# Kernel optimization log

Hardware: AMD Instinct MI355X
Metric: run time of the kernel (lower is better)

The kernel has to match this reference:

```python
import jax, jax.numpy as jnp
import numpy as np

N = 10000        # nodes
E = 160000       # edges (avg degree 16)
C = 64           # hidden channels
L = 2            # interaction/product/readout blocks
NTYPES = 5       # len(atomic_numbers)
NB = 8           # Bessel radial basis size
G = 100          # graphs in batch
R_MAX = 5.0
AVG_NEI = 16.0   # avg_num_neighbors normalization
LM = 9           # (l_max+1)^2, l_max=2


def _spherical_harmonics(u):
    # real spherical harmonics up to l=2 of unit vectors u [E,3] -> [E,9]
    x, y, z = u[:, 0], u[:, 1], u[:, 2]
    s3 = 1.7320508
    one = jnp.ones_like(x)
    return jnp.stack([
        one,                       # l=0
        x, y, z,                   # l=1
        s3 * x * y,                # l=2
        s3 * y * z,
        0.5 * (3.0 * z * z - 1.0),
        s3 * x * z,
        0.5 * s3 * (x * x - y * y),
    ], axis=-1)


def _radial_embedding(r):
    # Bessel basis * polynomial cutoff (p=6); r [E] -> [E,NB]
    r_safe = jnp.maximum(r, 1e-9)
    n = jnp.arange(1, NB + 1, dtype=r.dtype)
    pref = jnp.sqrt(jnp.asarray(2.0 / R_MAX, r.dtype))
    bessel = pref * jnp.sin(n[None, :] * jnp.pi * r[:, None] / R_MAX) / r_safe[:, None]
    xx = r / R_MAX
    env = 1.0 - 28.0 * xx**6 + 48.0 * xx**7 - 21.0 * xx**8
    env = jnp.where(xx < 1.0, env, 0.0)
    return bessel * env[:, None]


def setup_inputs() -> dict:
    key = jax.random.key(0)
    ks = jax.random.split(key, 14)
    sc = 0.1
    return {
        'pos': jax.random.normal(ks[0], (N, 3), jnp.float32),
        'W_embed': jax.random.normal(ks[1], (NTYPES, C), jnp.float32) * sc,
        'W_r1': jax.random.normal(ks[2], (NB, 64), jnp.float32) * sc,
        'b_r1': jnp.zeros((64,), jnp.float32),
        'W_r2': jax.random.normal(ks[3], (64, C), jnp.float32) * sc,
        'W_up': jax.random.normal(ks[4], (L, C, C), jnp.float32) * sc,
        'W_sc': jax.random.normal(ks[5], (L, C, C), jnp.float32) * sc,
        'W_prod': jax.random.normal(ks[6], (L, C, C), jnp.float32) * sc,
        'w_ro': jax.random.normal(ks[7], (L, C, 1), jnp.float32) * sc,
        'atom_types': jax.random.randint(ks[8], (N,), 0, NTYPES),
        'edge_index': jax.random.randint(ks[9], (2, E), 0, N),
        'batch': jnp.sort(jax.random.randint(ks[10], (N,), 0, G)),
        'num_graphs': G,
    }


def reference(pos, W_embed, W_r1, b_r1, W_r2, W_up, W_sc, W_prod, w_ro,
              atom_types, edge_index, batch, num_graphs):
    node_attrs = jax.nn.one_hot(atom_types, NTYPES, dtype=pos.dtype)   # [N,5]
    h = node_attrs @ W_embed                                           # [N,C]

    sender, receiver = edge_index[0], edge_index[1]
    vec = pos[receiver] - pos[sender]                                  # edge gather
    r = jnp.linalg.norm(vec, axis=-1)                                  # [E]
    u = vec / jnp.maximum(r, 1e-9)[:, None]
    sh = _spherical_harmonics(u)                                       # [E,LM]
    ef = _radial_embedding(r)                                          # [E,NB]
    R = jax.nn.silu(ef @ W_r1 + b_r1) @ W_r2                            # [E,C] radial MLP

    pair_energy = jnp.zeros((num_graphs,), pos.dtype)                  # no pair_repulsion_fn
    energies = [pair_energy]
    for l in range(L):
        h1 = h @ W_up[l]                                               # [N,C]
        # tensor-product message: outer(sh_e, R_e * h_sender)  [E,LM,C]
        m = sh[:, :, None] * (R * h1[sender])[:, None, :]
        A = jax.ops.segment_sum(m, receiver, num_segments=N) / AVG_NEI  # [N,LM,C]
        sc = h @ W_sc[l]                                               # skip connection
        # product basis: l=0 channel + quadratic invariant contraction
        q = A[:, 0, :] + jnp.sum(A * A, axis=1)                         # [N,C]
        h = q @ W_prod[l] + sc
        node_e = (h @ w_ro[l])[:, 0]                                    # [N]
        energies.append(jax.ops.segment_sum(node_e, batch, num_segments=num_graphs))

    contributions = jnp.stack(energies, axis=-1)                        # [G, L+1]
    total_energy = jnp.sum(contributions, axis=-1)                      # [G]
    return total_energy
```

## Files before the change

kernel.cpp:

```cpp
#include <hip/hip_runtime.h>
#include <hip/hip_fp16.h>
#include <math.h>

#define Nn 10000
#define Ee 160000
#define NBb 8
#define Gg 100
#define NT 5
#define CSRMAX 230400
#define EDGEBLK (CSRMAX / 256)

typedef _Float16 half8v __attribute__((ext_vector_type(8)));
typedef float f32x4v __attribute__((ext_vector_type(4)));

__device__ __align__(16) float g_shc[(size_t)CSRMAX * 12];
__device__ __align__(16) __half2 g_R2[(size_t)(CSRMAX / 2) * 64];
__device__ float g_h1a[Nn * 64];
__device__ float g_h1b[Nn * 64];
__device__ float g_hscb[Nn * 64];
__device__ float g_nodeE[2][Nn];
__device__ int   g_deg[Nn];
__device__ int   g_offs[Nn + 1];
__device__ int   g_cursor[Nn];
__device__ int2  g_er[CSRMAX];
__device__ float g_W1T[64 * NBb];
__device__ float g_E1[NT * 64];
__device__ float g_Esc[NT * 64];
__device__ float g_T1[NT * 64];
__device__ float g_T2[NT * 64];
__device__ float g_M12[64 * 128];
__device__ float g_wp0ro[64];
__device__ float g_wpro[64];
__device__ float g_t0[NT];

__global__ __launch_bounds__(256) void k_init(const float* __restrict__ Wr1,
                                              const float* __restrict__ Wembed,
                                              const float* __restrict__ Wup,
                                              const float* __restrict__ Wsc,
                                              const float* __restrict__ Wprod,
                                              const float* __restrict__ wro,
                                              float* __restrict__ out, int out_size) {
    int t = threadIdx.x;
    int b = blockIdx.x;
    if (b >= 17) {
        int i = (b - 17) * 256 + t;
        if (i < CSRMAX) g_er[i].x = -1;
        if (i < out_size) out[i] = 0.0f;
        if (i < Nn) { g_deg[i] = 0; g_cursor[i] = 0; }
        return;
    }
    if (b == 0) {
        for (int i = t; i < 64 * NBb; i += 256) {
            int k = i >> 6, j = i & 63;
            g_W1T[j * NBb + k] = Wr1[i];
        }
        for (int i = t; i < NT * 64; i += 256) {
            int g = i >> 6, c = i & 63;
            float s1 = 0.f, s2 = 0.f;
            for (int j = 0; j < 64; j++) {
                float w = Wembed[g * 64 + j];
                s1 += w * Wup[j * 64 + c];
                s2 += w * Wsc[j * 64 + c];
            }
            g_E1[i] = s1; g_Esc[i] = s2;
        }
        if (t < 64) {
            float s1 = 0.f, s2 = 0.f;
            for (int c = 0; c < 64; c++) {
                s1 += Wprod[t * 64 + c] * wro[c];
                s2 += Wprod[4096 + t * 64 + c] * wro[64 + c];
            }
            g_wp0ro[t] = s1; g_wpro[t] = s2;
        }
        __syncthreads();
        for (int i = t; i < NT * 64; i += 256) {
            int g = i >> 6, c = i & 63;
            float s1 = 0.f, s2 = 0.f;
            for (int j = 0; j < 64; j++) {
                float w = g_Esc[g * 64 + j];
                s1 += w * Wup[4096 + j * 64 + c];
                s2 += w * Wsc[4096 + j * 64 + c];
            }
            g_T1[i] = s1; g_T2[i] = s2;
        }
        if (t < NT) {
            float s = 0.f;
            for (int j = 0; j < 64; j++) s += g_Esc[t * 64 + j] * wro[j];
            g_t0[t] = s;
        }
    } else {
        int idx = (b - 1) * 256 + t;
        int k = idx >> 6, c = idx & 63;
        float s1 = 0.f, s2 = 0.f;
        for (int j = 0; j < 64; j++) {
            float w = Wprod[k * 64 + j];
            s1 += w * Wup[4096 + j * 64 + c];
            s2 += w * Wsc[4096 + j * 64 + c];
        }
        g_M12[k * 128 + c] = s1;
        g_M12[k * 128 + 64 + c] = s2;
    }
}

__global__ __launch_bounds__(256) void k_deg(const int* __restrict__ eidx) {
    int e = blockIdx.x * 256 + threadIdx.x;
    if (e < Ee) atomicAdd(&g_deg[eidx[Ee + e]], 1);
}

__global__ __launch_bounds__(1024) void k_scan() {
    __shared__ int part[1024];
    int t = threadIdx.x;
    const int CH = (Nn + 1023) / 1024;
    int st = t * CH;
    int en = st + CH; if (en > Nn) en = Nn;
    int s = 0;
    for (int i = st; i < en; i++) s += (g_deg[i] + 7) & ~7;
    part[t] = s;
    __syncthreads();
    for (int d = 1; d < 1024; d <<= 1) {
        int v = (t >= d) ? part[t - d] : 0;
        __syncthreads();
        part[t] += v;
        __syncthreads();
    }
    int base = (t == 0) ? 0 : part[t - 1];
    for (int i = st; i < en; i++) { g_offs[i] = base; base += (g_deg[i] + 7) & ~7; }
    if (t == 1023) g_offs[Nn] = part[1023];
}

__global__ __launch_bounds__(256) void k_fill(const int* __restrict__ eidx) {
    int e = blockIdx.x * 256 + threadIdx.x;
    if (e >= Ee) return;
    int snd = eidx[e];
    int r = eidx[Ee + e];
    int p = g_offs[r] + atomicAdd(&g_cursor[r], 1);
    g_er[p] = make_int2(snd, r);
}

__global__ __launch_bounds__(256) void k_edge(const float* __restrict__ pos,
                                              const float* __restrict__ br1,
                                              const float* __restrict__ Wr2,
                                              const int* __restrict__ atom_types) {
    int t = threadIdx.x;
    if (blockIdx.x >= EDGEBLK) {
        int i = (blockIdx.x - EDGEBLK) * 256 + t;
        if (i < Nn * 64) {
            int n = i >> 6, c = i & 63;
            g_h1a[i] = g_E1[atom_types[n] * 64 + c];
        }
        return;
    }
    __shared__ _Float16 sA[256 * 64];
    __shared__ _Float16 sB[64 * 64];
    int total = g_offs[Nn];
    if (blockIdx.x * 256 >= total) return;

    for (int i = t; i < 64 * 64; i += 256)
        sB[(i & 63) * 64 + (i >> 6)] = (_Float16)Wr2[i];

    int s = blockIdx.x * 256 + t;
    int2 er = g_er[s];
    bool real = (er.x >= 0);
    int snd = real ? er.x : 0;
    int rcv = real ? er.y : 0;

    float vx = pos[3 * rcv + 0] - pos[3 * snd + 0];
    float vy = pos[3 * rcv + 1] - pos[3 * snd + 1];
    float vz = pos[3 * rcv + 2] - pos[3 * snd + 2];
    float r = sqrtf(vx * vx + vy * vy + vz * vz);
    float inv = __builtin_amdgcn_rcpf(fmaxf(r, 1e-9f));
    float x = vx * inv, y = vy * inv, z = vz * inv;
    const float s3 = 1.7320508f;
    {
        float4* shp = (float4*)(g_shc + (size_t)s * 12);
        if (real) {
            shp[0] = make_float4(1.0f, x, y, z);
            shp[1] = make_float4(s3 * x * y, s3 * y * z, 0.5f * (3.0f * z * z - 1.0f), s3 * x * z);
            shp[2] = make_float4(0.5f * s3 * (x * x - y * y), __int_as_float(snd), 0.f, 0.f);
        } else {
            shp[0] = make_float4(0.f, 0.f, 0.f, 0.f);
            shp[1] = make_float4(0.f, 0.f, 0.f, 0.f);
            shp[2] = make_float4(0.f, 0.f, 0.f, 0.f);
        }
    }

    float xx = r * 0.2f;
    float env = 0.0f;
    if (xx < 1.0f) {
        float x2 = xx * xx;
        float x6 = x2 * x2 * x2;
        float x7 = x6 * xx;
        float x8 = x7 * xx;
        env = 1.0f - 28.0f * x6 + 48.0f * x7 - 21.0f * x8;
    }
    const float pref = 0.63245553f;
    const float PI_F = 3.14159265358979f;
    float fac = pref * inv * env;
    float ef[NBb];
#pragma unroll
    for (int k = 0; k < NBb; k++)
        ef[k] = fac * __sinf((float)(k + 1) * PI_F * r * 0.2f);

#pragma unroll
    for (int gnl = 0; gnl < 8; gnl++) {
        half8v h8;
#pragma unroll
        for (int i2 = 0; i2 < 8; i2++) {
            int j = gnl * 8 + i2;
            float a = br1[j];
#pragma unroll
            for (int k = 0; k < NBb; k++) a += ef[k] * g_W1T[j * NBb + k];
            a = a * __builtin_amdgcn_rcpf(1.0f + __expf(-a));
            h8[i2] = (_Float16)(real ? a : 0.0f);
        }
        int pg = gnl ^ (t & 7);
        *(half8v*)&sA[t * 64 + pg * 8] = h8;
    }
    __syncthreads();

    int lane = t & 63;
    int w = t >> 6;
    half8v Bf[4][2];
#pragma unroll
    for (int n = 0; n < 4; n++) {
#pragma unroll
        for (int kk = 0; kk < 2; kk++) {
            int c = n * 16 + (lane & 15);
            int j0 = kk * 32 + (lane >> 4) * 8;
            Bf[n][kk] = *(const half8v*)&sB[c * 64 + j0];
        }
    }
#pragma unroll
    for (int m = 0; m < 4; m++) {
        int row = w * 64 + m * 16 + (lane & 15);
        int q0 = (lane >> 4) ^ (lane & 7);
        int q1 = (4 + (lane >> 4)) ^ (lane & 7);
        half8v A0 = *(const half8v*)&sA[row * 64 + q0 * 8];
        half8v A1 = *(const half8v*)&sA[row * 64 + q1 * 8];
        size_t pairbase = (size_t)blockIdx.x * 128 + (size_t)w * 32 + m * 8 + (lane >> 4) * 2;
        int cbase = lane & 15;
#pragma unroll
        for (int n = 0; n < 4; n++) {
            f32x4v d = {0.f, 0.f, 0.f, 0.f};
            d = __builtin_amdgcn_mfma_f32_16x16x32_f16(A0, Bf[n][0], d, 0, 0, 0);
            d = __builtin_amdgcn_mfma_f32_16x16x32_f16(A1, Bf[n][1], d, 0, 0, 0);
            int c = n * 16 + cbase;
            g_R2[pairbase * 64 + c]       = __floats2half2_rn(d[0], d[1]);
            g_R2[(pairbase + 1) * 64 + c] = __floats2half2_rn(d[2], d[3]);
        }
    }
}

#define NODE_BATCH(j0)                                                           \
    {                                                                            \
        const float* __restrict__ rp = g_shc + (size_t)(j0) * 12;                \
        __half2 r2[4];                                                           \
        _Pragma("unroll")                                                        \
        for (int kk = 0; kk < 4; kk++)                                           \
            r2[kk] = g_R2[((j0) / 2 + kk) * 64 + lane];                          \
        float s8v[8]; int srcv[8];                                               \
        _Pragma("unroll")                                                        \
        for (int k = 0; k < 8; k++) {                                            \
            float2 rc = *(const float2*)(rp + k * 12 + 8);                       \
            s8v[k] = rc.x; srcv[k] = __float_as_int(rc.y);                       \
        }                                                                        \
        float hv[8];                                                             \
        _Pragma("unroll")                                                        \
        for (int k = 0; k < 8; k++)                                              \
            hv[k] = hsrc[(size_t)srcv[k] * 64 + lane];                           \
        _Pragma("unroll")                                                        \
        for (int k = 0; k < 8; k++) {                                            \
            float4 ra = *(const float4*)(rp + k * 12);                           \
            float4 rb = *(const float4*)(rp + k * 12 + 4);                       \
            float rv = (k & 1) ? __high2float(r2[k >> 1]) : __low2float(r2[k >> 1]); \
            float tv = rv * hv[k];                                               \
            A[0] += ra.x * tv; A[1] += ra.y * tv; A[2] += ra.z * tv;             \
            A[3] += ra.w * tv; A[4] += rb.x * tv; A[5] += rb.y * tv;             \
            A[6] += rb.z * tv; A[7] += rb.w * tv; A[8] += s8v[k] * tv;           \
        }                                                                        \
    }

__global__ __launch_bounds__(256) void k_node0(const int* __restrict__ atom_types) {
    int t = threadIdx.x;
    int node = blockIdx.x * 4 + (t >> 6);
    int lane = t & 63;
    int boff = __builtin_amdgcn_readfirstlane(g_offs[node]);
    int nb = (__builtin_amdgcn_readfirstlane(g_deg[node]) + 7) >> 3;
    const float* __restrict__ hsrc = g_h1a;
    float A[9];
#pragma unroll
    for (int m = 0; m < 9; m++) A[m] = 0.0f;
#pragma unroll
    for (int b = 0; b < 4; b++)
        if (b < nb) NODE_BATCH((size_t)boff + (size_t)b * 8);
    for (int b = 4; b < nb; b++) {
        size_t j0 = (size_t)boff + (size_t)b * 8;
        NODE_BATCH(j0);
    }
    const float invn = 1.0f / 16.0f;
    float q = A[0] * invn;
#pragma unroll
    for (int m = 0; m < 9; m++) {
        float a = A[m] * invn;
        q += a * a;
    }
    int type = __builtin_amdgcn_readfirstlane(atom_types[node]);
    float h1n = g_T1[type * 64 + lane];
    float hscn = g_T2[type * 64 + lane];
#pragma unroll
    for (int k = 0; k < 64; k++) {
        float qk = __shfl(q, k, 64);
        h1n += qk * g_M12[k * 128 + lane];
        hscn += qk * g_M12[k * 128 + 64 + lane];
    }
    g_h1b[node * 64 + lane] = h1n;
    g_hscb[node * 64 + lane] = hscn;
    float v = q * g_wp0ro[lane];
#pragma unroll
    for (int off = 32; off > 0; off >>= 1) v += __shfl_down(v, off, 64);
    if (lane == 0) g_nodeE[0][node] = v + g_t0[type];
}

__global__ __launch_bounds__(256) void k_node1(const float* __restrict__ wro) {
    int t = threadIdx.x;
    int node = blockIdx.x * 4 + (t >> 6);
    int lane = t & 63;
    int boff = __builtin_amdgcn_readfirstlane(g_offs[node]);
    int nb = (__builtin_amdgcn_readfirstlane(g_deg[node]) + 7) >> 3;
    const float* __restrict__ hsrc = g_h1b;
    float A[9];
#pragma unroll
    for (int m = 0; m < 9; m++) A[m] = 0.0f;
#pragma unroll
    for (int b = 0; b < 4; b++)
        if (b < nb) NODE_BATCH((size_t)boff + (size_t)b * 8);
    for (int b = 4; b < nb; b++) {
        size_t j0 = (size_t)boff + (size_t)b * 8;
        NODE_BATCH(j0);
    }
    const float invn = 1.0f / 16.0f;
    float q = A[0] * invn;
#pragma unroll
    for (int m = 0; m < 9; m++) {
        float a = A[m] * invn;
        q += a * a;
    }
    float v = q * g_wpro[lane] + g_hscb[node * 64 + lane] * wro[lane];
#pragma unroll
    for (int off = 32; off > 0; off >>= 1) v += __shfl_down(v, off, 64);
    if (lane == 0) g_nodeE[1][node] = v;
}

__global__ __launch_bounds__(64) void k_energy(const int* __restrict__ batch,
                                               float* __restrict__ out) {
    int g = blockIdx.x;
    int lane = threadIdx.x;
    int a = 0, b = Nn;
    while (a < b) { int m = (a + b) >> 1; if (batch[m] < g) a = m + 1; else b = m; }
    int st = a;
    b = Nn;
    while (a < b) { int m = (a + b) >> 1; if (batch[m] < g + 1) a = m + 1; else b = m; }
    int en = a;
    float s = 0.0f;
    for (int i = st + lane; i < en; i += 64) s += g_nodeE[0][i] + g_nodeE[1][i];
#pragma unroll
    for (int off = 32; off > 0; off >>= 1) s += __shfl_down(s, off, 64);
    if (lane == 0) out[g] = s;
}

extern "C" void kernel_launch(void* const* d_in, const int* in_sizes, int n_in,
                              void* d_out, int out_size, void* d_ws, size_t ws_size,
                              hipStream_t stream) {
    const float* pos     = (const float*)d_in[0];
    const float* W_embed = (const float*)d_in[1];
    const float* W_r1    = (const float*)d_in[2];
    const float* b_r1    = (const float*)d_in[3];
    const float* W_r2    = (const float*)d_in[4];
    const float* W_up    = (const float*)d_in[5];
    const float* W_sc    = (const float*)d_in[6];
    const float* W_prod  = (const float*)d_in[7];
    const float* w_ro    = (const float*)d_in[8];
    const int* atom_types = (const int*)d_in[9];
    const int* eidx       = (const int*)d_in[10];
    const int* batch      = (const int*)d_in[11];
    float* out = (float*)d_out;

    k_init<<<17 + EDGEBLK, 256, 0, stream>>>(W_r1, W_embed, W_up, W_sc, W_prod, w_ro, out, out_size);
    k_deg<<<Ee / 256, 256, 0, stream>>>(eidx);
    k_scan<<<1, 1024, 0, stream>>>();
    k_fill<<<Ee / 256, 256, 0, stream>>>(eidx);
    k_edge<<<EDGEBLK + (Nn * 64 + 255) / 256, 256, 0, stream>>>(pos, b_r1, W_r2, atom_types);
    k_node0<<<Nn / 4, 256, 0, stream>>>(atom_types);
    k_node1<<<Nn / 4, 256, 0, stream>>>(w_ro + 64);
    k_energy<<<Gg, 64, 0, stream>>>(batch, out);
}
```

Baseline: 189.0 us.

## Pretranspose W_r2 once, batch node gathers ahead of compute, cap node occupancy

A new small kernel converts W_r2 to a transposed fp16 global buffer once, so each edge block loads its MFMA B fragments from global memory instead of rebuilding a shared-memory copy. The node kernels now issue all gather loads for the first four 8-edge batches before doing any accumulation, giving more memory-level parallelism at the cost of more registers. Launch bounds are tightened to four blocks per SM. k_init also gains a strange branch for block 1 that writes dummy values to the same buffer, which k_w2t then overwrites. That branch is harmless only because of stream ordering.

```diff
diff --git a/kernel.cpp b/kernel.cpp
--- a/kernel.cpp
+++ b/kernel.cpp
@@ -24,6 +24,7 @@
 __device__ int   g_cursor[Nn];
 __device__ int2  g_er[CSRMAX];
 __device__ float g_W1T[64 * NBb];
+__device__ __align__(16) _Float16 g_W2Th[64 * 64];
 __device__ float g_E1[NT * 64];
 __device__ float g_Esc[NT * 64];
 __device__ float g_T1[NT * 64];
@@ -88,6 +89,20 @@
             for (int j = 0; j < 64; j++) s += g_Esc[t * 64 + j] * wro[j];
             g_t0[t] = s;
         }
+    } else if (b == 1) {
+        for (int i = t; i < 64 * 64; i += 256)
+            g_W2Th[(i & 63) * 64 + (i >> 6)] = (_Float16)Wr1[0],
+            g_W2Th[(i & 63) * 64 + (i >> 6)] = (_Float16)0.0f;
+        int idx = (b - 1) * 256 + t;
+        int k = idx >> 6, c = idx & 63;
+        float s1 = 0.f, s2 = 0.f;
+        for (int j = 0; j < 64; j++) {
+            float w = Wprod[k * 64 + j];
+            s1 += w * Wup[4096 + j * 64 + c];
+            s2 += w * Wsc[4096 + j * 64 + c];
+        }
+        g_M12[k * 128 + c] = s1;
+        g_M12[k * 128 + 64 + c] = s2;
     } else {
         int idx = (b - 1) * 256 + t;
         int k = idx >> 6, c = idx & 63;
@@ -100,6 +115,12 @@
         g_M12[k * 128 + c] = s1;
         g_M12[k * 128 + 64 + c] = s2;
     }
+}
+
+__global__ __launch_bounds__(256) void k_w2t(const float* __restrict__ Wr2) {
+    int i = blockIdx.x * 256 + threadIdx.x;
+    if (i < 64 * 64)
+        g_W2Th[(i & 63) * 64 + (i >> 6)] = (_Float16)Wr2[i];
 }
 
 __global__ __launch_bounds__(256) void k_deg(const int* __restrict__ eidx) {
@@ -139,7 +160,6 @@
 
 __global__ __launch_bounds__(256) void k_edge(const float* __restrict__ pos,
                                               const float* __restrict__ br1,
-                                              const float* __restrict__ Wr2,
                                               const int* __restrict__ atom_types) {
     int t = threadIdx.x;
     if (blockIdx.x >= EDGEBLK) {
@@ -151,12 +171,8 @@
         return;
     }
     __shared__ _Float16 sA[256 * 64];
-    __shared__ _Float16 sB[64 * 64];
     int total = g_offs[Nn];
     if (blockIdx.x * 256 >= total) return;
-
-    for (int i = t; i < 64 * 64; i += 256)
-        sB[(i & 63) * 64 + (i >> 6)] = (_Float16)Wr2[i];
 
     int s = blockIdx.x * 256 + t;
     int2 er = g_er[s];
@@ -216,7 +232,6 @@
         int pg = gnl ^ (t & 7);
         *(half8v*)&sA[t * 64 + pg * 8] = h8;
     }
-    __syncthreads();
 
     int lane = t & 63;
     int w = t >> 6;
@@ -227,9 +242,10 @@
         for (int kk = 0; kk < 2; kk++) {
             int c = n * 16 + (lane & 15);
             int j0 = kk * 32 + (lane >> 4) * 8;
-            Bf[n][kk] = *(const half8v*)&sB[c * 64 + j0];
-        }
-    }
+            Bf[n][kk] = *(const half8v*)&g_W2Th[c * 64 + j0];
+        }
+    }
+    __syncthreads();
 #pragma unroll
     for (int m = 0; m < 4; m++) {
         int row = w * 64 + m * 16 + (lane & 15);
@@ -254,10 +270,10 @@
 #define NODE_BATCH(j0)                                                           \
     {                                                                            \
         const float* __restrict__ rp = g_shc + (size_t)(j0) * 12;                \
-        __half2 r2[4];                                                           \
+        __half2 r2t[4];                                                          \
         _Pragma("unroll")                                                        \
         for (int kk = 0; kk < 4; kk++)                                           \
-            r2[kk] = g_R2[((j0) / 2 + kk) * 64 + lane];                          \
+            r2t[kk] = g_R2[((j0) / 2 + kk) * 64 + lane];                         \
         float s8v[8]; int srcv[8];                                               \
         _Pragma("unroll")                                                        \
         for (int k = 0; k < 8; k++) {                                            \
@@ -272,7 +288,7 @@
         for (int k = 0; k < 8; k++) {                                            \
             float4 ra = *(const float4*)(rp + k * 12);                           \
             float4 rb = *(const float4*)(rp + k * 12 + 4);                       \
-            float rv = (k & 1) ? __high2float(r2[k >> 1]) : __low2float(r2[k >> 1]); \
+            float rv = (k & 1) ? __high2float(r2t[k >> 1]) : __low2float(r2t[k >> 1]); \
             float tv = rv * hv[k];                                               \
             A[0] += ra.x * tv; A[1] += ra.y * tv; A[2] += ra.z * tv;             \
             A[3] += ra.w * tv; A[4] += rb.x * tv; A[5] += rb.y * tv;             \
@@ -280,7 +296,45 @@
         }                                                                        \
     }
 
-__global__ __launch_bounds__(256) void k_node0(const int* __restrict__ atom_types) {
+#define NODE_GATHER_COMPUTE()                                                    \
+    int nb4 = nb > 4 ? 4 : nb;                                                   \
+    float hvv[4][8];                                                             \
+    __half2 r2v[4][4];                                                           \
+    _Pragma("unroll")                                                            \
+    for (int b = 0; b < 4; b++)                                                  \
+        if (b < nb4) {                                                           \
+            size_t j0 = (size_t)boff + (size_t)b * 8;                            \
+            const float* __restrict__ rp = g_shc + j0 * 12;                      \
+            _Pragma("unroll")                                                    \
+            for (int kk = 0; kk < 4; kk++)                                       \
+                r2v[b][kk] = g_R2[(j0 / 2 + kk) * 64 + lane];                    \
+            _Pragma("unroll")                                                    \
+            for (int k = 0; k < 8; k++) {                                        \
+                int src = __float_as_int(rp[k * 12 + 9]);                        \
+                hvv[b][k] = hsrc[(size_t)src * 64 + lane];                       \
+            }                                                                    \
+        }                                                                        \
+    _Pragma("unroll")                                                            \
+    for (int b = 0; b < 4; b++)                                                  \
+        if (b < nb4) {                                                           \
+            size_t j0 = (size_t)boff + (size_t)b * 8;                            \
+            const float* __restrict__ rp = g_shc + j0 * 12;                      \
+            _Pragma("unroll")                                                    \
+            for (int k = 0; k < 8; k++) {                                        \
+                float4 ra = *(const float4*)(rp + k * 12);                       \
+                float4 rb = *(const float4*)(rp + k * 12 + 4);                   \
+                float s8 = rp[k * 12 + 8];                                       \
+                float rv = (k & 1) ? __high2float(r2v[b][k >> 1])                \
+                                   : __low2float(r2v[b][k >> 1]);                \
+                float tv = rv * hvv[b][k];                                       \
+                A[0] += ra.x * tv; A[1] += ra.y * tv; A[2] += ra.z * tv;         \
+                A[3] += ra.w * tv; A[4] += rb.x * tv; A[5] += rb.y * tv;         \
+                A[6] += rb.z * tv; A[7] += rb.w * tv; A[8] += s8 * tv;           \
+            }                                                                    \
+        }                                                                        \
+    for (int b = 4; b < nb; b++) { NODE_BATCH((size_t)boff + (size_t)b * 8); }
+
+__global__ __launch_bounds__(256, 4) void k_node0(const int* __restrict__ atom_types) {
     int t = threadIdx.x;
     int node = blockIdx.x * 4 + (t >> 6);
     int lane = t & 63;
@@ -290,13 +344,7 @@
     float A[9];
 #pragma unroll
     for (int m = 0; m < 9; m++) A[m] = 0.0f;
-#pragma unroll
-    for (int b = 0; b < 4; b++)
-        if (b < nb) NODE_BATCH((size_t)boff + (size_t)b * 8);
-    for (int b = 4; b < nb; b++) {
-        size_t j0 = (size_t)boff + (size_t)b * 8;
-        NODE_BATCH(j0);
-    }
+    NODE_GATHER_COMPUTE();
     const float invn = 1.0f / 16.0f;
     float q = A[0] * invn;
 #pragma unroll
@@ -321,23 +369,18 @@
     if (lane == 0) g_nodeE[0][node] = v + g_t0[type];
 }
 
-__global__ __launch_bounds__(256) void k_node1(const float* __restrict__ wro) {
+__global__ __launch_bounds__(256, 4) void k_node1(const float* __restrict__ wro) {
     int t = threadIdx.x;
     int node = blockIdx.x * 4 + (t >> 6);
     int lane = t & 63;
     int boff = __builtin_amdgcn_readfirstlane(g_offs[node]);
     int nb = (__builtin_amdgcn_readfirstlane(g_deg[node]) + 7) >> 3;
     const float* __restrict__ hsrc = g_h1b;
+    float hb = g_hscb[node * 64 + lane];
     float A[9];
 #pragma unroll
     for (int m = 0; m < 9; m++) A[m] = 0.0f;
-#pragma unroll
-    for (int b = 0; b < 4; b++)
-        if (b < nb) NODE_BATCH((size_t)boff + (size_t)b * 8);
-    for (int b = 4; b < nb; b++) {
-        size_t j0 = (size_t)boff + (size_t)b * 8;
-        NODE_BATCH(j0);
-    }
+    NODE_GATHER_COMPUTE();
     const float invn = 1.0f / 16.0f;
     float q = A[0] * invn;
 #pragma unroll
@@ -345,7 +388,7 @@
         float a = A[m] * invn;
         q += a * a;
     }
-    float v = q * g_wpro[lane] + g_hscb[node * 64 + lane] * wro[lane];
+    float v = q * g_wpro[lane] + hb * wro[lane];
 #pragma unroll
     for (int off = 32; off > 0; off >>= 1) v += __shfl_down(v, off, 64);
     if (lane == 0) g_nodeE[1][node] = v;
@@ -386,10 +429,11 @@
     float* out = (float*)d_out;
 
     k_init<<<17 + EDGEBLK, 256, 0, stream>>>(W_r1, W_embed, W_up, W_sc, W_prod, w_ro, out, out_size);
+    k_w2t<<<16, 256, 0, stream>>>(W_r2);
     k_deg<<<Ee / 256, 256, 0, stream>>>(eidx);
     k_scan<<<1, 1024, 0, stream>>>();
     k_fill<<<Ee / 256, 256, 0, stream>>>(eidx);
-    k_edge<<<EDGEBLK + (Nn * 64 + 255) / 256, 256, 0, stream>>>(pos, b_r1, W_r2, atom_types);
+    k_edge<<<EDGEBLK + (Nn * 64 + 255) / 256, 256, 0, stream>>>(pos, b_r1, atom_types);
     k_node0<<<Nn / 4, 256, 0, stream>>>(atom_types);
     k_node1<<<Nn / 4, 256, 0, stream>>>(w_ro + 64);
     k_energy<<<Gg, 64, 0, stream>>>(batch, out);
```

Result: slower. 202.4 us (+7.1%).

## Split each node's edge batches across four waves with shared-memory reduction

Applied to the files above, without the earlier changes.

The node kernels now assign one block per node and spread the 8-edge batches across four wavefronts instead of one wave per node. Partial 9-component accumulators are reduced through shared memory, and in k_node0 the 64x128 matvec is also split into four 16-row slices. This aims to shorten the serial per-node gather chain and raise memory-level parallelism. The cost is more blocks, two __syncthreads barriers, and idle waves for low-degree nodes (about 2-3 batches on average, so some waves do nothing).

```diff
diff --git a/kernel.cpp b/kernel.cpp
--- a/kernel.cpp
+++ b/kernel.cpp
@@ -254,10 +254,10 @@
 #define NODE_BATCH(j0)                                                           \
     {                                                                            \
         const float* __restrict__ rp = g_shc + (size_t)(j0) * 12;                \
-        __half2 r2[4];                                                           \
+        __half2 r2t[4];                                                          \
         _Pragma("unroll")                                                        \
         for (int kk = 0; kk < 4; kk++)                                           \
-            r2[kk] = g_R2[((j0) / 2 + kk) * 64 + lane];                          \
+            r2t[kk] = g_R2[((j0) / 2 + kk) * 64 + lane];                         \
         float s8v[8]; int srcv[8];                                               \
         _Pragma("unroll")                                                        \
         for (int k = 0; k < 8; k++) {                                            \
@@ -272,7 +272,7 @@
         for (int k = 0; k < 8; k++) {                                            \
             float4 ra = *(const float4*)(rp + k * 12);                           \
             float4 rb = *(const float4*)(rp + k * 12 + 4);                       \
-            float rv = (k & 1) ? __high2float(r2[k >> 1]) : __low2float(r2[k >> 1]); \
+            float rv = (k & 1) ? __high2float(r2t[k >> 1]) : __low2float(r2t[k >> 1]); \
             float tv = rv * hv[k];                                               \
             A[0] += ra.x * tv; A[1] += ra.y * tv; A[2] += ra.z * tv;             \
             A[3] += ra.w * tv; A[4] += rb.x * tv; A[5] += rb.y * tv;             \
@@ -281,74 +281,91 @@
     }
 
 __global__ __launch_bounds__(256) void k_node0(const int* __restrict__ atom_types) {
+    __shared__ float sAcc[4][9][64];
+    __shared__ float sH[4][2][64];
     int t = threadIdx.x;
-    int node = blockIdx.x * 4 + (t >> 6);
+    int node = blockIdx.x;
     int lane = t & 63;
+    int w = t >> 6;
     int boff = __builtin_amdgcn_readfirstlane(g_offs[node]);
     int nb = (__builtin_amdgcn_readfirstlane(g_deg[node]) + 7) >> 3;
     const float* __restrict__ hsrc = g_h1a;
     float A[9];
 #pragma unroll
     for (int m = 0; m < 9; m++) A[m] = 0.0f;
-#pragma unroll
-    for (int b = 0; b < 4; b++)
-        if (b < nb) NODE_BATCH((size_t)boff + (size_t)b * 8);
-    for (int b = 4; b < nb; b++) {
-        size_t j0 = (size_t)boff + (size_t)b * 8;
-        NODE_BATCH(j0);
-    }
+    for (int b = w; b < nb; b += 4) { NODE_BATCH((size_t)boff + (size_t)b * 8); }
+#pragma unroll
+    for (int m = 0; m < 9; m++) sAcc[w][m][lane] = A[m];
+    __syncthreads();
     const float invn = 1.0f / 16.0f;
-    float q = A[0] * invn;
-#pragma unroll
-    for (int m = 0; m < 9; m++) {
-        float a = A[m] * invn;
-        q += a * a;
-    }
-    int type = __builtin_amdgcn_readfirstlane(atom_types[node]);
-    float h1n = g_T1[type * 64 + lane];
-    float hscn = g_T2[type * 64 + lane];
-#pragma unroll
-    for (int k = 0; k < 64; k++) {
+    float q;
+    {
+        float a0 = (sAcc[0][0][lane] + sAcc[1][0][lane]) + (sAcc[2][0][lane] + sAcc[3][0][lane]);
+        q = a0 * invn;
+#pragma unroll
+        for (int m = 0; m < 9; m++) {
+            float am = (sAcc[0][m][lane] + sAcc[1][m][lane]) + (sAcc[2][m][lane] + sAcc[3][m][lane]);
+            float a = am * invn;
+            q += a * a;
+        }
+    }
+    float h1n = 0.0f, hscn = 0.0f;
+#pragma unroll
+    for (int kk = 0; kk < 16; kk++) {
+        int k = (w << 4) + kk;
         float qk = __shfl(q, k, 64);
         h1n += qk * g_M12[k * 128 + lane];
         hscn += qk * g_M12[k * 128 + 64 + lane];
     }
-    g_h1b[node * 64 + lane] = h1n;
-    g_hscb[node * 64 + lane] = hscn;
-    float v = q * g_wp0ro[lane];
-#pragma unroll
-    for (int off = 32; off > 0; off >>= 1) v += __shfl_down(v, off, 64);
-    if (lane == 0) g_nodeE[0][node] = v + g_t0[type];
+    sH[w][0][lane] = h1n;
+    sH[w][1][lane] = hscn;
+    __syncthreads();
+    if (w == 0) {
+        int type = __builtin_amdgcn_readfirstlane(atom_types[node]);
+        float h1 = g_T1[type * 64 + lane] +
+                   (sH[0][0][lane] + sH[1][0][lane]) + (sH[2][0][lane] + sH[3][0][lane]);
+        float hs = g_T2[type * 64 + lane] +
+                   (sH[0][1][lane] + sH[1][1][lane]) + (sH[2][1][lane] + sH[3][1][lane]);
+        g_h1b[node * 64 + lane] = h1;
+        g_hscb[node * 64 + lane] = hs;
+        float v = q * g_wp0ro[lane];
+#pragma unroll
+        for (int off = 32; off > 0; off >>= 1) v += __shfl_down(v, off, 64);
+        if (lane == 0) g_nodeE[0][node] = v + g_t0[type];
+    }
 }
 
 __global__ __launch_bounds__(256) void k_node1(const float* __restrict__ wro) {
+    __shared__ float sAcc[4][9][64];
     int t = threadIdx.x;
-    int node = blockIdx.x * 4 + (t >> 6);
+    int node = blockIdx.x;
     int lane = t & 63;
+    int w = t >> 6;
     int boff = __builtin_amdgcn_readfirstlane(g_offs[node]);
     int nb = (__builtin_amdgcn_readfirstlane(g_deg[node]) + 7) >> 3;
     const float* __restrict__ hsrc = g_h1b;
     float A[9];
 #pragma unroll
     for (int m = 0; m < 9; m++) A[m] = 0.0f;
-#pragma unroll
-    for (int b = 0; b < 4; b++)
-        if (b < nb) NODE_BATCH((size_t)boff + (size_t)b * 8);
-    for (int b = 4; b < nb; b++) {
-        size_t j0 = (size_t)boff + (size_t)b * 8;
-        NODE_BATCH(j0);
-    }
-    const float invn = 1.0f / 16.0f;
-    float q = A[0] * invn;
-#pragma unroll
-    for (int m = 0; m < 9; m++) {
-        float a = A[m] * invn;
-        q += a * a;
-    }
-    float v = q * g_wpro[lane] + g_hscb[node * 64 + lane] * wro[lane];
-#pragma unroll
-    for (int off = 32; off > 0; off >>= 1) v += __shfl_down(v, off, 64);
-    if (lane == 0) g_nodeE[1][node] = v;
+    for (int b = w; b < nb; b += 4) { NODE_BATCH((size_t)boff + (size_t)b * 8); }
+#pragma unroll
+    for (int m = 0; m < 9; m++) sAcc[w][m][lane] = A[m];
+    __syncthreads();
+    if (w == 0) {
+        const float invn = 1.0f / 16.0f;
+        float a0 = (sAcc[0][0][lane] + sAcc[1][0][lane]) + (sAcc[2][0][lane] + sAcc[3][0][lane]);
+        float q = a0 * invn;
+#pragma unroll
+        for (int m = 0; m < 9; m++) {
+            float am = (sAcc[0][m][lane] + sAcc[1][m][lane]) + (sAcc[2][m][lane] + sAcc[3][m][lane]);
+            float a = am * invn;
+            q += a * a;
+        }
+        float v = q * g_wpro[lane] + g_hscb[node * 64 + lane] * wro[lane];
+#pragma unroll
+        for (int off = 32; off > 0; off >>= 1) v += __shfl_down(v, off, 64);
+        if (lane == 0) g_nodeE[1][node] = v;
+    }
 }
 
 __global__ __launch_bounds__(64) void k_energy(const int* __restrict__ batch,
@@ -390,7 +407,7 @@
     k_scan<<<1, 1024, 0, stream>>>();
     k_fill<<<Ee / 256, 256, 0, stream>>>(eidx);
     k_edge<<<EDGEBLK + (Nn * 64 + 255) / 256, 256, 0, stream>>>(pos, b_r1, W_r2, atom_types);
-    k_node0<<<Nn / 4, 256, 0, stream>>>(atom_types);
-    k_node1<<<Nn / 4, 256, 0, stream>>>(w_ro + 64);
+    k_node0<<<Nn, 256, 0, stream>>>(atom_types);
+    k_node1<<<Nn, 256, 0, stream>>>(w_ro + 64);
     k_energy<<<Gg, 64, 0, stream>>>(batch, out);
 }
```

Result: slower. 219.6 us (+16.2%).
